# Kernel tuning notes

Measured on AMD Instinct MI355X. Metric: run time of the kernel, lower is better.

## Reference

```python
import jax, jax.numpy as jnp
import numpy as np

# Dimensions: D must equal C_CHUNK**2 (original code's view+transpose requires it)
D = 4096        # flattened input dim per sample
C_CHUNK = 64    # chunk_size (rows of G per chunk)
N_CHUNKS = D // C_CHUNK  # = 64
H = 512         # hidden dim of forward_func MLP
C_OUT = 8       # output classes of forward_func
B = 8           # batch size (state_batch has 2*B rows)
EPS_G = 1e-4    # metric regularizer (constant under grad)


def setup_inputs() -> dict:
    key = jax.random.key(0)
    ks = jax.random.split(key, 6)
    t = jax.random.uniform(ks[0], (1,), dtype=jnp.float32)
    state_batch = jax.random.normal(ks[1], (2 * B, D), dtype=jnp.float32)
    x0_batch = jax.random.normal(ks[2], (B, D), dtype=jnp.float32)
    x1_batch = jax.random.normal(ks[3], (B, D), dtype=jnp.float32)
    W1 = jax.random.normal(ks[4], (D, H), dtype=jnp.float32) / np.float32(np.sqrt(D))
    W2 = jax.random.normal(ks[5], (H, C_OUT), dtype=jnp.float32) / np.float32(np.sqrt(H))
    return {"t": t, "state_batch": state_batch, "x0_batch": x0_batch,
            "x1_batch": x1_batch, "W1": W1, "W2": W2}


def _accel_per_sample(x, v, W1, W2):
    """Chunked Christoffel-symbol contraction for one sample.
    x: [D] current point, v: [D] deviation velocity. Returns a: [D]."""
    def f(xi):  # forward_func: 2-layer tanh MLP, [D] -> [C_OUT]
        return jnp.tanh(xi @ W1) @ W2

    ones = jnp.ones((D,), x.dtype)

    def chunk_sums(xi):
        # G = J^T J + eps*I; row_sums[i] = sum_j G[i,j] computed without
        # materializing the D x D metric: J^T (J @ 1)  (+ const eps on diag).
        J = jax.jacrev(f)(xi)              # [C_OUT, D]
        row = J.T @ (J @ ones)             # [D]
        return row.reshape(N_CHUNKS, C_CHUNK).sum(axis=1)  # [N_CHUNKS]

    g = jax.jacrev(chunk_sums)(x)          # [N_CHUNKS, D] = dG_chunk_sum/dx
    g = g.reshape(N_CHUNKS, C_CHUNK, C_CHUNK)
    g = g / (jnp.linalg.norm(g, axis=2, keepdims=True) + 1e-6)
    Gamma = 0.5 * (g + jnp.swapaxes(g, 1, 2))   # symmetrized [nc, c, c]
    vc = v.reshape(N_CHUNKS, C_CHUNK)
    # a_chunk[i] = -sum_k Gamma[i,k] v_i v_k  (Christoffel quadratic in v)
    a = -jnp.einsum('nik,ni,nk->ni', Gamma, vc, vc)
    return a.reshape(D)


def reference(t, state_batch, x0_batch, x1_batch, W1, W2):
    ts = t[0]
    Bn = state_batch.shape[0] // 2
    deviation = state_batch[:Bn]
    dev_velocity = state_batch[Bn:]
    window = 4.0 * ts * (1.0 - ts)
    x = x0_batch + ts * (x1_batch - x0_batch) + window * deviation  # [B, D]
    a = jax.vmap(_accel_per_sample, in_axes=(0, 0, None, None))(x, dev_velocity, W1, W2)
    a = a / (jnp.linalg.norm(dev_velocity, axis=1, keepdims=True) + 1e-6)
    restoration = -0.1 * deviation
    return jnp.concatenate([dev_velocity, a + restoration], axis=0)  # [2B, D]
```

## Files before the change

### kernel.cpp

```cpp
#include <hip/hip_runtime.h>

#define D 4096
#define H 512
#define NCH 64
#define CCH 64
#define B 8
#define COUT 8

typedef __bf16 bf16x8 __attribute__((ext_vector_type(8)));
typedef float  f32x4  __attribute__((ext_vector_type(4)));

#define OFF_P    0
#define OFF_PHN  (OFF_P + NCH*H)
#define OFF_UPT  (OFF_PHN + H*NCH)
#define OFF_S    (OFF_UPT + B*H*NCH)
#define OFF_ST2  (OFF_S + B*H)
#define OFF_Q    (OFF_ST2 + B*H)
#define OFF_C    (OFF_Q + B*H)
#define OFF_VN   (OFF_C + H)
#define OFF_A1   (OFF_VN + 64)
#define OFF_ZB   (OFF_A1 + B*NCH*CCH)
#define OFF_W1H  (OFF_ZB + B*64*4096)
#define OFF_W1L  (OFF_W1H + (D*H)/2)
#define OFF_WH   (OFF_W1L + (D*H)/2)
#define OFF_WL   (OFF_WH + (B*NCH*H)/2)

__device__ __forceinline__ unsigned short f2bf(float x) {
    unsigned int u = __float_as_uint(x);
    unsigned int r = (u + 0x7FFFu + ((u >> 16) & 1u)) >> 16;
    return (unsigned short)r;
}
__device__ __forceinline__ float bf2f(unsigned short s) {
    return __uint_as_float(((unsigned int)s) << 16);
}

__global__ __launch_bounds__(256) void k1_reduce_w1(const float* __restrict__ W1,
                                                    const float* __restrict__ state,
                                                    const float* __restrict__ x0,
                                                    const float* __restrict__ x1,
                                                    const float* __restrict__ tptr,
                                                    float* __restrict__ ws) {
    int n   = blockIdx.x;
    int ht  = blockIdx.y;
    int tid = threadIdx.x;
    int hq  = ht * 32 + (tid & 31);
    int jh  = tid >> 5;

    __shared__ float xs[B][64];
    __shared__ f32x4 red[8][32][9];

    float ts = tptr[0];
    float window = 4.f * ts * (1.f - ts);
    if (tid < 64) {
        int d = n * 64 + tid;
        for (int b = 0; b < B; ++b) {
            float a0 = x0[b * D + d];
            float a1v = x1[b * D + d];
            float dev = state[b * D + d];
            xs[b][tid] = a0 + ts * (a1v - a0) + window * dev;
        }
    }
    __syncthreads();

    unsigned short* __restrict__ W1Hp = (unsigned short*)(ws + OFF_W1H);
    unsigned short* __restrict__ W1Lp = (unsigned short*)(ws + OFF_W1L);

    f32x4 p4 = {0.f, 0.f, 0.f, 0.f};
    f32x4 up[B];
#pragma unroll
    for (int b = 0; b < B; ++b) up[b] = p4;

#pragma unroll
    for (int jj = 0; jj < 8; ++jj) {
        int j = jh * 8 + jj;
        int d = n * 64 + j;
        f32x4 w = ((const f32x4*)W1)[d * (H / 4) + hq];
        p4 += w;
#pragma unroll
        for (int b = 0; b < B; ++b) up[b] += w * xs[b][j];
        unsigned short h0 = f2bf(w.x), h1 = f2bf(w.y), h2 = f2bf(w.z), h3 = f2bf(w.w);
        ushort4 hv = {h0, h1, h2, h3};
        ushort4 lv = {f2bf(w.x - bf2f(h0)), f2bf(w.y - bf2f(h1)),
                      f2bf(w.z - bf2f(h2)), f2bf(w.w - bf2f(h3))};
        *(ushort4*)(W1Hp + d * H + hq * 4) = hv;
        *(ushort4*)(W1Lp + d * H + hq * 4) = lv;
    }

    int l = tid & 31;
    red[jh][l][0] = p4;
#pragma unroll
    for (int b = 0; b < B; ++b) red[jh][l][1 + b] = up[b];
    __syncthreads();

    if (jh == 0) {
        f32x4 pt = red[0][l][0];
        f32x4 ut[B];
#pragma unroll
        for (int b = 0; b < B; ++b) ut[b] = red[0][l][1 + b];
        for (int g = 1; g < 8; ++g) {
            pt += red[g][l][0];
#pragma unroll
            for (int b = 0; b < B; ++b) ut[b] += red[g][l][1 + b];
        }
        *(f32x4*)(ws + OFF_P + n * H + hq * 4) = pt;
#pragma unroll
        for (int e = 0; e < 4; ++e) ws[OFF_PHN + (hq * 4 + e) * NCH + n] = pt[e];
#pragma unroll
        for (int b = 0; b < B; ++b)
#pragma unroll
            for (int e = 0; e < 4; ++e)
                ws[OFF_UPT + (b * H + hq * 4 + e) * NCH + n] = ut[b][e];
    }
}

__global__ void k2_sample(const float* __restrict__ W2,
                          const float* __restrict__ state,
                          float* __restrict__ ws) {
    int b = blockIdx.x, tid = threadIdx.x;
    int wid = tid >> 6, lane = tid & 63;
    __shared__ float lm[8][8];
    __shared__ float ms[8];
    __shared__ float lv[8];

    int h = tid;
    f32x4 u4 = {0.f, 0.f, 0.f, 0.f}, c4 = u4;
    const f32x4* upp = (const f32x4*)(ws + OFF_UPT + (b * H + h) * NCH);
    const f32x4* pp  = (const f32x4*)(ws + OFF_PHN + h * NCH);
#pragma unroll
    for (int j = 0; j < 16; ++j) { u4 += upp[j]; c4 += pp[j]; }
    float u = u4.x + u4.y + u4.z + u4.w;
    float c = c4.x + c4.y + c4.z + c4.w;

    float tt  = tanhf(u);
    float s   = 1.f - tt * tt;
    float st2 = -2.f * tt * s;
    ws[OFF_S   + b * H + h] = s;
    ws[OFF_ST2 + b * H + h] = st2;
    ws[OFF_C   + h] = c;

    const float4* w2p = (const float4*)(W2 + h * 8);
    float4 w2a = w2p[0], w2b = w2p[1];
    float w2r[8] = {w2a.x, w2a.y, w2a.z, w2a.w, w2b.x, w2b.y, w2b.z, w2b.w};

    float cs = c * s;
    float pr[8];
#pragma unroll
    for (int o = 0; o < 8; ++o) pr[o] = cs * w2r[o];
#pragma unroll
    for (int mk = 1; mk < 64; mk <<= 1)
#pragma unroll
        for (int o = 0; o < 8; ++o) pr[o] += __shfl_xor(pr[o], mk);
    if (lane == 0)
#pragma unroll
        for (int o = 0; o < 8; ++o) lm[wid][o] = pr[o];

    float v2 = 0.f;
    const float* v = state + (size_t)(B + b) * D;
#pragma unroll
    for (int j = 0; j < D / H; ++j) { float vv = v[j * H + h]; v2 += vv * vv; }
#pragma unroll
    for (int mk = 1; mk < 64; mk <<= 1) v2 += __shfl_xor(v2, mk);
    if (lane == 0) lv[wid] = v2;
    __syncthreads();

    if (tid < 8) {
        float a = 0.f;
        for (int w = 0; w < 8; ++w) a += lm[w][tid];
        ms[tid] = a;
    }
    if (tid == 0) {
        float a = 0.f;
        for (int w = 0; w < 8; ++w) a += lv[w];
        ws[OFF_VN + b] = sqrtf(a) + 1e-6f;
    }
    __syncthreads();

    float q = 0.f;
#pragma unroll
    for (int o = 0; o < 8; ++o) q += w2r[o] * ms[o];
    ws[OFF_Q + b * H + h] = q;
}

__global__ void k3_w(const float* __restrict__ W2,
                     float* __restrict__ ws) {
    int n = blockIdx.x, b = blockIdx.y, lane = threadIdx.x;
    float M[8];
#pragma unroll
    for (int o = 0; o < 8; ++o) M[o] = 0.f;
    for (int j = 0; j < 8; ++j) {
        int h = j * 64 + lane;
        float ps = ws[OFF_P + n * H + h] * ws[OFF_S + b * H + h];
        const float4* wp = (const float4*)(W2 + h * 8);
        float4 wa = wp[0], wb = wp[1];
        M[0] += ps * wa.x; M[1] += ps * wa.y; M[2] += ps * wa.z; M[3] += ps * wa.w;
        M[4] += ps * wb.x; M[5] += ps * wb.y; M[6] += ps * wb.z; M[7] += ps * wb.w;
    }
#pragma unroll
    for (int mk = 1; mk < 64; mk <<= 1)
#pragma unroll
        for (int o = 0; o < 8; ++o) M[o] += __shfl_xor(M[o], mk);

    unsigned short* __restrict__ WHp = (unsigned short*)(ws + OFF_WH);
    unsigned short* __restrict__ WLp = (unsigned short*)(ws + OFF_WL);
    for (int j = 0; j < 8; ++j) {
        int h = j * 64 + lane;
        const float4* wp = (const float4*)(W2 + h * 8);
        float4 wa = wp[0], wb = wp[1];
        float r = wa.x*M[0] + wa.y*M[1] + wa.z*M[2] + wa.w*M[3]
                + wb.x*M[4] + wb.y*M[5] + wb.z*M[6] + wb.w*M[7];
        float P = ws[OFF_P + n * H + h];
        float wv = ws[OFF_ST2 + b * H + h] * (P * ws[OFF_Q + b * H + h] + ws[OFF_C + h] * r);
        unsigned short hi = f2bf(wv);
        WHp[(b * NCH + n) * H + h] = hi;
        WLp[(b * NCH + n) * H + h] = f2bf(wv - bf2f(hi));
    }
}

__global__ __launch_bounds__(256) void k4_mfma(const float* __restrict__ state,
                                               float* __restrict__ ws) {
    int i   = blockIdx.x;
    int b   = blockIdx.y;
    int tid = threadIdx.x;
    int wid = tid >> 6, lane = tid & 63;
    int r16 = lane & 15;
    int kgrp = (lane >> 4) * 8;

    __shared__ float gp[2][64][67];
    __shared__ float coefs[64];

    const unsigned short* __restrict__ W1Hp = (const unsigned short*)(ws + OFF_W1H);
    const unsigned short* __restrict__ W1Lp = (const unsigned short*)(ws + OFF_W1L);
    const unsigned short* __restrict__ WHp  = (const unsigned short*)(ws + OFF_WH);
    const unsigned short* __restrict__ WLp  = (const unsigned short*)(ws + OFF_WL);

    f32x4 acc[4][4];
    f32x4 z4 = {0.f, 0.f, 0.f, 0.f};
#pragma unroll
    for (int m = 0; m < 4; ++m)
#pragma unroll
        for (int c = 0; c < 4; ++c) acc[m][c] = z4;

    int kb = wid * 128 + kgrp;
#pragma unroll
    for (int ks = 0; ks < 4; ++ks) {
        int k = kb + ks * 32;
        bf16x8 ah[4], al[4], bh[4], bl[4];
#pragma unroll
        for (int m = 0; m < 4; ++m) {
            int off = (b * 64 + m * 16 + r16) * H + k;
            ah[m] = *(const bf16x8*)(WHp + off);
            al[m] = *(const bf16x8*)(WLp + off);
        }
#pragma unroll
        for (int c = 0; c < 4; ++c) {
            int off = (i * 64 + c * 16 + r16) * H + k;
            bh[c] = *(const bf16x8*)(W1Hp + off);
            bl[c] = *(const bf16x8*)(W1Lp + off);
        }
#pragma unroll
        for (int m = 0; m < 4; ++m)
#pragma unroll
            for (int c = 0; c < 4; ++c) {
                acc[m][c] = __builtin_amdgcn_mfma_f32_16x16x32_bf16(ah[m], bh[c], acc[m][c], 0, 0, 0);
                acc[m][c] = __builtin_amdgcn_mfma_f32_16x16x32_bf16(ah[m], bl[c], acc[m][c], 0, 0, 0);
                acc[m][c] = __builtin_amdgcn_mfma_f32_16x16x32_bf16(al[m], bh[c], acc[m][c], 0, 0, 0);
            }
    }

    int rowb = (lane >> 4) * 4;
    if (wid < 2) {
        float (*g)[67] = gp[wid];
#pragma unroll
        for (int m = 0; m < 4; ++m)
#pragma unroll
            for (int c = 0; c < 4; ++c)
#pragma unroll
                for (int e = 0; e < 4; ++e)
                    g[m * 16 + rowb + e][c * 16 + r16] = acc[m][c][e];
    }
    __syncthreads();
    if (wid >= 2) {
        float (*g)[67] = gp[wid - 2];
#pragma unroll
        for (int m = 0; m < 4; ++m)
#pragma unroll
            for (int c = 0; c < 4; ++c)
#pragma unroll
                for (int e = 0; e < 4; ++e)
                    g[m * 16 + rowb + e][c * 16 + r16] += acc[m][c][e];
    }
    __syncthreads();

    const float* v = state + (size_t)(B + b) * D;

    if (tid < 64) {
        int n = tid;
        float ss = 0.f, y = 0.f;
#pragma unroll 8
        for (int k = 0; k < 64; ++k) {
            float g = gp[0][n][k] + gp[1][n][k];
            ss += g * g;
            y  += g * v[n * 64 + k];
        }
        float nrm = sqrtf(ss) + 1e-6f;
        ws[OFF_A1 + (size_t)(b * NCH + n) * CCH + i] = y / nrm;
        coefs[n] = v[n * 64 + i] / nrm;
    }
    __syncthreads();

    float* zb = ws + OFF_ZB + ((size_t)b * 64 + i) * 4096;
#pragma unroll
    for (int r = 0; r < 16; ++r) {
        int idx = tid + r * 256;
        int n = idx >> 6, k = idx & 63;
        zb[idx] = (gp[0][n][k] + gp[1][n][k]) * coefs[n];
    }
}

__global__ void k5_final(const float* __restrict__ state,
                         const float* __restrict__ ws,
                         float* __restrict__ out) {
    int idx = blockIdx.x * 256 + threadIdx.x;
    float vel = state[32768 + idx];
    out[idx] = vel;
    int b = idx >> 12, e = idx & 4095;
    const float* zb = ws + OFF_ZB + (size_t)b * 64 * 4096 + e;
    float z = 0.f;
#pragma unroll 8
    for (int i = 0; i < 64; ++i) z += zb[(size_t)i * 4096];
    float a1 = ws[OFF_A1 + (size_t)b * 4096 + e];
    float av = -0.5f * vel * (a1 + z) / ws[OFF_VN + b];
    out[32768 + idx] = av - 0.1f * state[idx];
}

extern "C" void kernel_launch(void* const* d_in, const int* in_sizes, int n_in,
                              void* d_out, int out_size, void* d_ws, size_t ws_size,
                              hipStream_t stream) {
    const float* t   = (const float*)d_in[0];
    const float* st  = (const float*)d_in[1];
    const float* x0  = (const float*)d_in[2];
    const float* x1  = (const float*)d_in[3];
    const float* W1  = (const float*)d_in[4];
    const float* W2  = (const float*)d_in[5];
    float* out = (float*)d_out;
    float* ws  = (float*)d_ws;

    hipLaunchKernelGGL(k1_reduce_w1, dim3(64, 4), dim3(256), 0, stream, W1, st, x0, x1, t, ws);
    hipLaunchKernelGGL(k2_sample,    dim3(8),     dim3(512), 0, stream, W2, st, ws);
    hipLaunchKernelGGL(k3_w,         dim3(64, 8), dim3(64),  0, stream, W2, ws);
    hipLaunchKernelGGL(k4_mfma,      dim3(64, 8), dim3(256), 0, stream, st, ws);
    hipLaunchKernelGGL(k5_final,     dim3(128),   dim3(256), 0, stream, st, ws, out);
}
```

Before: 121.8 us.

## Fuse five kernels into one cooperative kernel with grid syncs

```diff
diff --git a/kernel.cpp b/kernel.cpp
--- a/kernel.cpp
+++ b/kernel.cpp
@@ -1,11 +1,13 @@
 #include <hip/hip_runtime.h>
+#include <hip/hip_cooperative_groups.h>
+
+namespace cg = cooperative_groups;
 
 #define D 4096
 #define H 512
 #define NCH 64
 #define CCH 64
 #define B 8
-#define COUT 8
 
 typedef __bf16 bf16x8 __attribute__((ext_vector_type(8)));
 typedef float  f32x4  __attribute__((ext_vector_type(4)));
@@ -34,303 +36,310 @@
     return __uint_as_float(((unsigned int)s) << 16);
 }
 
-__global__ __launch_bounds__(256) void k1_reduce_w1(const float* __restrict__ W1,
-                                                    const float* __restrict__ state,
-                                                    const float* __restrict__ x0,
-                                                    const float* __restrict__ x1,
-                                                    const float* __restrict__ tptr,
-                                                    float* __restrict__ ws) {
-    int n   = blockIdx.x;
-    int ht  = blockIdx.y;
+__global__ __launch_bounds__(512, 2)
+void fused(const float* __restrict__ W1, const float* __restrict__ state,
+           const float* __restrict__ x0, const float* __restrict__ x1,
+           const float* __restrict__ tptr, const float* __restrict__ W2,
+           float* __restrict__ ws, float* __restrict__ out) {
+    cg::grid_group grid = cg::this_grid();
+    int bid = blockIdx.x;
     int tid = threadIdx.x;
-    int hq  = ht * 32 + (tid & 31);
-    int jh  = tid >> 5;
-
-    __shared__ float xs[B][64];
-    __shared__ f32x4 red[8][32][9];
-
-    float ts = tptr[0];
-    float window = 4.f * ts * (1.f - ts);
-    if (tid < 64) {
-        int d = n * 64 + tid;
-        for (int b = 0; b < B; ++b) {
-            float a0 = x0[b * D + d];
-            float a1v = x1[b * D + d];
-            float dev = state[b * D + d];
-            xs[b][tid] = a0 + ts * (a1v - a0) + window * dev;
-        }
-    }
-    __syncthreads();
+
+    __shared__ union {
+        struct { float xs[B][64]; f32x4 red[8][32][9]; } p1;
+        struct { float lm[8][8]; float ms[8]; float lv[8]; } p2;
+        struct { float gp[2][2][64][67]; float coefs[2][64]; } p4;
+    } sh;
 
     unsigned short* __restrict__ W1Hp = (unsigned short*)(ws + OFF_W1H);
     unsigned short* __restrict__ W1Lp = (unsigned short*)(ws + OFF_W1L);
-
-    f32x4 p4 = {0.f, 0.f, 0.f, 0.f};
-    f32x4 up[B];
-#pragma unroll
-    for (int b = 0; b < B; ++b) up[b] = p4;
-
-#pragma unroll
-    for (int jj = 0; jj < 8; ++jj) {
-        int j = jh * 8 + jj;
-        int d = n * 64 + j;
-        f32x4 w = ((const f32x4*)W1)[d * (H / 4) + hq];
-        p4 += w;
-#pragma unroll
-        for (int b = 0; b < B; ++b) up[b] += w * xs[b][j];
-        unsigned short h0 = f2bf(w.x), h1 = f2bf(w.y), h2 = f2bf(w.z), h3 = f2bf(w.w);
-        ushort4 hv = {h0, h1, h2, h3};
-        ushort4 lv = {f2bf(w.x - bf2f(h0)), f2bf(w.y - bf2f(h1)),
-                      f2bf(w.z - bf2f(h2)), f2bf(w.w - bf2f(h3))};
-        *(ushort4*)(W1Hp + d * H + hq * 4) = hv;
-        *(ushort4*)(W1Lp + d * H + hq * 4) = lv;
-    }
-
-    int l = tid & 31;
-    red[jh][l][0] = p4;
-#pragma unroll
-    for (int b = 0; b < B; ++b) red[jh][l][1 + b] = up[b];
-    __syncthreads();
-
-    if (jh == 0) {
-        f32x4 pt = red[0][l][0];
-        f32x4 ut[B];
-#pragma unroll
-        for (int b = 0; b < B; ++b) ut[b] = red[0][l][1 + b];
-        for (int g = 1; g < 8; ++g) {
-            pt += red[g][l][0];
-#pragma unroll
-            for (int b = 0; b < B; ++b) ut[b] += red[g][l][1 + b];
-        }
-        *(f32x4*)(ws + OFF_P + n * H + hq * 4) = pt;
-#pragma unroll
-        for (int e = 0; e < 4; ++e) ws[OFF_PHN + (hq * 4 + e) * NCH + n] = pt[e];
-#pragma unroll
-        for (int b = 0; b < B; ++b)
-#pragma unroll
-            for (int e = 0; e < 4; ++e)
-                ws[OFF_UPT + (b * H + hq * 4 + e) * NCH + n] = ut[b][e];
-    }
-}
-
-__global__ void k2_sample(const float* __restrict__ W2,
-                          const float* __restrict__ state,
-                          float* __restrict__ ws) {
-    int b = blockIdx.x, tid = threadIdx.x;
-    int wid = tid >> 6, lane = tid & 63;
-    __shared__ float lm[8][8];
-    __shared__ float ms[8];
-    __shared__ float lv[8];
-
-    int h = tid;
-    f32x4 u4 = {0.f, 0.f, 0.f, 0.f}, c4 = u4;
-    const f32x4* upp = (const f32x4*)(ws + OFF_UPT + (b * H + h) * NCH);
-    const f32x4* pp  = (const f32x4*)(ws + OFF_PHN + h * NCH);
-#pragma unroll
-    for (int j = 0; j < 16; ++j) { u4 += upp[j]; c4 += pp[j]; }
-    float u = u4.x + u4.y + u4.z + u4.w;
-    float c = c4.x + c4.y + c4.z + c4.w;
-
-    float tt  = tanhf(u);
-    float s   = 1.f - tt * tt;
-    float st2 = -2.f * tt * s;
-    ws[OFF_S   + b * H + h] = s;
-    ws[OFF_ST2 + b * H + h] = st2;
-    ws[OFF_C   + h] = c;
-
-    const float4* w2p = (const float4*)(W2 + h * 8);
-    float4 w2a = w2p[0], w2b = w2p[1];
-    float w2r[8] = {w2a.x, w2a.y, w2a.z, w2a.w, w2b.x, w2b.y, w2b.z, w2b.w};
-
-    float cs = c * s;
-    float pr[8];
-#pragma unroll
-    for (int o = 0; o < 8; ++o) pr[o] = cs * w2r[o];
-#pragma unroll
-    for (int mk = 1; mk < 64; mk <<= 1)
-#pragma unroll
-        for (int o = 0; o < 8; ++o) pr[o] += __shfl_xor(pr[o], mk);
-    if (lane == 0)
-#pragma unroll
-        for (int o = 0; o < 8; ++o) lm[wid][o] = pr[o];
-
-    float v2 = 0.f;
-    const float* v = state + (size_t)(B + b) * D;
-#pragma unroll
-    for (int j = 0; j < D / H; ++j) { float vv = v[j * H + h]; v2 += vv * vv; }
-#pragma unroll
-    for (int mk = 1; mk < 64; mk <<= 1) v2 += __shfl_xor(v2, mk);
-    if (lane == 0) lv[wid] = v2;
-    __syncthreads();
-
-    if (tid < 8) {
-        float a = 0.f;
-        for (int w = 0; w < 8; ++w) a += lm[w][tid];
-        ms[tid] = a;
-    }
-    if (tid == 0) {
-        float a = 0.f;
-        for (int w = 0; w < 8; ++w) a += lv[w];
-        ws[OFF_VN + b] = sqrtf(a) + 1e-6f;
-    }
-    __syncthreads();
-
-    float q = 0.f;
-#pragma unroll
-    for (int o = 0; o < 8; ++o) q += w2r[o] * ms[o];
-    ws[OFF_Q + b * H + h] = q;
-}
-
-__global__ void k3_w(const float* __restrict__ W2,
-                     float* __restrict__ ws) {
-    int n = blockIdx.x, b = blockIdx.y, lane = threadIdx.x;
-    float M[8];
-#pragma unroll
-    for (int o = 0; o < 8; ++o) M[o] = 0.f;
-    for (int j = 0; j < 8; ++j) {
-        int h = j * 64 + lane;
-        float ps = ws[OFF_P + n * H + h] * ws[OFF_S + b * H + h];
-        const float4* wp = (const float4*)(W2 + h * 8);
-        float4 wa = wp[0], wb = wp[1];
-        M[0] += ps * wa.x; M[1] += ps * wa.y; M[2] += ps * wa.z; M[3] += ps * wa.w;
-        M[4] += ps * wb.x; M[5] += ps * wb.y; M[6] += ps * wb.z; M[7] += ps * wb.w;
-    }
-#pragma unroll
-    for (int mk = 1; mk < 64; mk <<= 1)
-#pragma unroll
-        for (int o = 0; o < 8; ++o) M[o] += __shfl_xor(M[o], mk);
-
-    unsigned short* __restrict__ WHp = (unsigned short*)(ws + OFF_WH);
-    unsigned short* __restrict__ WLp = (unsigned short*)(ws + OFF_WL);
-    for (int j = 0; j < 8; ++j) {
-        int h = j * 64 + lane;
-        const float4* wp = (const float4*)(W2 + h * 8);
-        float4 wa = wp[0], wb = wp[1];
-        float r = wa.x*M[0] + wa.y*M[1] + wa.z*M[2] + wa.w*M[3]
-                + wb.x*M[4] + wb.y*M[5] + wb.z*M[6] + wb.w*M[7];
-        float P = ws[OFF_P + n * H + h];
-        float wv = ws[OFF_ST2 + b * H + h] * (P * ws[OFF_Q + b * H + h] + ws[OFF_C + h] * r);
-        unsigned short hi = f2bf(wv);
-        WHp[(b * NCH + n) * H + h] = hi;
-        WLp[(b * NCH + n) * H + h] = f2bf(wv - bf2f(hi));
-    }
-}
-
-__global__ __launch_bounds__(256) void k4_mfma(const float* __restrict__ state,
-                                               float* __restrict__ ws) {
-    int i   = blockIdx.x;
-    int b   = blockIdx.y;
-    int tid = threadIdx.x;
-    int wid = tid >> 6, lane = tid & 63;
-    int r16 = lane & 15;
-    int kgrp = (lane >> 4) * 8;
-
-    __shared__ float gp[2][64][67];
-    __shared__ float coefs[64];
-
-    const unsigned short* __restrict__ W1Hp = (const unsigned short*)(ws + OFF_W1H);
-    const unsigned short* __restrict__ W1Lp = (const unsigned short*)(ws + OFF_W1L);
-    const unsigned short* __restrict__ WHp  = (const unsigned short*)(ws + OFF_WH);
-    const unsigned short* __restrict__ WLp  = (const unsigned short*)(ws + OFF_WL);
-
-    f32x4 acc[4][4];
-    f32x4 z4 = {0.f, 0.f, 0.f, 0.f};
-#pragma unroll
-    for (int m = 0; m < 4; ++m)
-#pragma unroll
-        for (int c = 0; c < 4; ++c) acc[m][c] = z4;
-
-    int kb = wid * 128 + kgrp;
-#pragma unroll
-    for (int ks = 0; ks < 4; ++ks) {
-        int k = kb + ks * 32;
-        bf16x8 ah[4], al[4], bh[4], bl[4];
-#pragma unroll
-        for (int m = 0; m < 4; ++m) {
-            int off = (b * 64 + m * 16 + r16) * H + k;
-            ah[m] = *(const bf16x8*)(WHp + off);
-            al[m] = *(const bf16x8*)(WLp + off);
-        }
-#pragma unroll
-        for (int c = 0; c < 4; ++c) {
-            int off = (i * 64 + c * 16 + r16) * H + k;
-            bh[c] = *(const bf16x8*)(W1Hp + off);
-            bl[c] = *(const bf16x8*)(W1Lp + off);
-        }
+    unsigned short* __restrict__ WHp  = (unsigned short*)(ws + OFF_WH);
+    unsigned short* __restrict__ WLp  = (unsigned short*)(ws + OFF_WL);
+
+    {
+        int n = bid >> 2, ht = bid & 3;
+        float ts = tptr[0];
+        float window = 4.f * ts * (1.f - ts);
+        if (tid < 64) {
+            int d = n * 64 + tid;
+            for (int b = 0; b < B; ++b) {
+                float a0 = x0[b * D + d];
+                float a1v = x1[b * D + d];
+                float dev = state[b * D + d];
+                sh.p1.xs[b][tid] = a0 + ts * (a1v - a0) + window * dev;
+            }
+        }
+        __syncthreads();
+
+        if (tid < 256) {
+            int hq = ht * 32 + (tid & 31);
+            int jh = tid >> 5;
+            f32x4 p4v = {0.f, 0.f, 0.f, 0.f};
+            f32x4 up[B];
+#pragma unroll
+            for (int b = 0; b < B; ++b) up[b] = p4v;
+#pragma unroll
+            for (int jj = 0; jj < 8; ++jj) {
+                int j = jh * 8 + jj;
+                int d = n * 64 + j;
+                f32x4 w = ((const f32x4*)W1)[d * (H / 4) + hq];
+                p4v += w;
+#pragma unroll
+                for (int b = 0; b < B; ++b) up[b] += w * sh.p1.xs[b][j];
+                unsigned short h0 = f2bf(w.x), h1 = f2bf(w.y), h2 = f2bf(w.z), h3 = f2bf(w.w);
+                ushort4 hv = {h0, h1, h2, h3};
+                ushort4 lv = {f2bf(w.x - bf2f(h0)), f2bf(w.y - bf2f(h1)),
+                              f2bf(w.z - bf2f(h2)), f2bf(w.w - bf2f(h3))};
+                *(ushort4*)(W1Hp + d * H + hq * 4) = hv;
+                *(ushort4*)(W1Lp + d * H + hq * 4) = lv;
+            }
+            int l = tid & 31;
+            sh.p1.red[jh][l][0] = p4v;
+#pragma unroll
+            for (int b = 0; b < B; ++b) sh.p1.red[jh][l][1 + b] = up[b];
+        }
+        __syncthreads();
+
+        if (tid < 32) {
+            int l = tid;
+            int hq = ht * 32 + l;
+            f32x4 pt = sh.p1.red[0][l][0];
+            f32x4 ut[B];
+#pragma unroll
+            for (int b = 0; b < B; ++b) ut[b] = sh.p1.red[0][l][1 + b];
+            for (int g = 1; g < 8; ++g) {
+                pt += sh.p1.red[g][l][0];
+#pragma unroll
+                for (int b = 0; b < B; ++b) ut[b] += sh.p1.red[g][l][1 + b];
+            }
+            *(f32x4*)(ws + OFF_P + n * H + hq * 4) = pt;
+#pragma unroll
+            for (int e = 0; e < 4; ++e) ws[OFF_PHN + (hq * 4 + e) * NCH + n] = pt[e];
+#pragma unroll
+            for (int b = 0; b < B; ++b)
+#pragma unroll
+                for (int e = 0; e < 4; ++e)
+                    ws[OFF_UPT + (b * H + hq * 4 + e) * NCH + n] = ut[b][e];
+        }
+    }
+    grid.sync();
+
+    if (bid < 8) {
+        int b = bid;
+        int wid = tid >> 6, lane = tid & 63;
+        int h = tid;
+        f32x4 u4 = {0.f, 0.f, 0.f, 0.f}, c4 = u4;
+        const f32x4* upp = (const f32x4*)(ws + OFF_UPT + (b * H + h) * NCH);
+        const f32x4* pp  = (const f32x4*)(ws + OFF_PHN + h * NCH);
+#pragma unroll
+        for (int j = 0; j < 16; ++j) { u4 += upp[j]; c4 += pp[j]; }
+        float u = u4.x + u4.y + u4.z + u4.w;
+        float c = c4.x + c4.y + c4.z + c4.w;
+
+        float tt  = tanhf(u);
+        float s   = 1.f - tt * tt;
+        float st2 = -2.f * tt * s;
+        ws[OFF_S   + b * H + h] = s;
+        ws[OFF_ST2 + b * H + h] = st2;
+        ws[OFF_C   + h] = c;
+
+        const float4* w2p = (const float4*)(W2 + h * 8);
+        float4 w2a = w2p[0], w2b = w2p[1];
+        float w2r[8] = {w2a.x, w2a.y, w2a.z, w2a.w, w2b.x, w2b.y, w2b.z, w2b.w};
+
+        float cs = c * s;
+        float pr[8];
+#pragma unroll
+        for (int o = 0; o < 8; ++o) pr[o] = cs * w2r[o];
+#pragma unroll
+        for (int mk = 1; mk < 64; mk <<= 1)
+#pragma unroll
+            for (int o = 0; o < 8; ++o) pr[o] += __shfl_xor(pr[o], mk);
+        if (lane == 0)
+#pragma unroll
+            for (int o = 0; o < 8; ++o) sh.p2.lm[wid][o] = pr[o];
+
+        float v2 = 0.f;
+        const float* v = state + (size_t)(B + b) * D;
+#pragma unroll
+        for (int j = 0; j < D / H; ++j) { float vv = v[j * H + h]; v2 += vv * vv; }
+#pragma unroll
+        for (int mk = 1; mk < 64; mk <<= 1) v2 += __shfl_xor(v2, mk);
+        if (lane == 0) sh.p2.lv[wid] = v2;
+        __syncthreads();
+
+        if (tid < 8) {
+            float a = 0.f;
+            for (int w = 0; w < 8; ++w) a += sh.p2.lm[w][tid];
+            sh.p2.ms[tid] = a;
+        }
+        if (tid == 0) {
+            float a = 0.f;
+            for (int w = 0; w < 8; ++w) a += sh.p2.lv[w];
+            ws[OFF_VN + b] = sqrtf(a) + 1e-6f;
+        }
+        __syncthreads();
+
+        float q = 0.f;
+#pragma unroll
+        for (int o = 0; o < 8; ++o) q += w2r[o] * sh.p2.ms[o];
+        ws[OFF_Q + b * H + h] = q;
+    }
+    grid.sync();
+
+    {
+        int gw = bid * 8 + (tid >> 6);
+        if (gw < 512) {
+            int n = gw >> 3, b = gw & 7;
+            int lane = tid & 63;
+            float M[8];
+#pragma unroll
+            for (int o = 0; o < 8; ++o) M[o] = 0.f;
+            for (int j = 0; j < 8; ++j) {
+                int h = j * 64 + lane;
+                float ps = ws[OFF_P + n * H + h] * ws[OFF_S + b * H + h];
+                const float4* wp = (const float4*)(W2 + h * 8);
+                float4 wa = wp[0], wb = wp[1];
+                M[0] += ps * wa.x; M[1] += ps * wa.y; M[2] += ps * wa.z; M[3] += ps * wa.w;
+                M[4] += ps * wb.x; M[5] += ps * wb.y; M[6] += ps * wb.z; M[7] += ps * wb.w;
+            }
+#pragma unroll
+            for (int mk = 1; mk < 64; mk <<= 1)
+#pragma unroll
+                for (int o = 0; o < 8; ++o) M[o] += __shfl_xor(M[o], mk);
+
+            for (int j = 0; j < 8; ++j) {
+                int h = j * 64 + lane;
+                const float4* wp = (const float4*)(W2 + h * 8);
+                float4 wa = wp[0], wb = wp[1];
+                float r = wa.x*M[0] + wa.y*M[1] + wa.z*M[2] + wa.w*M[3]
+                        + wb.x*M[4] + wb.y*M[5] + wb.z*M[6] + wb.w*M[7];
+                float P = ws[OFF_P + n * H + h];
+                float wv = ws[OFF_ST2 + b * H + h] * (P * ws[OFF_Q + b * H + h] + ws[OFF_C + h] * r);
+                unsigned short hi = f2bf(wv);
+                WHp[(b * NCH + n) * H + h] = hi;
+                WLp[(b * NCH + n) * H + h] = f2bf(wv - bf2f(hi));
+            }
+        }
+    }
+    grid.sync();
+
+    {
+        int g    = tid >> 8;
+        int gt   = tid & 255;
+        int u    = bid * 2 + g;
+        int i    = u >> 3, b = u & 7;
+        int w2   = gt >> 6;
+        int lane = tid & 63;
+        int r16  = lane & 15;
+        int kgrp = (lane >> 4) * 8;
+
+        f32x4 acc[4][4];
+        f32x4 zz = {0.f, 0.f, 0.f, 0.f};
 #pragma unroll
         for (int m = 0; m < 4; ++m)
 #pragma unroll
-            for (int c = 0; c < 4; ++c) {
-                acc[m][c] = __builtin_amdgcn_mfma_f32_16x16x32_bf16(ah[m], bh[c], acc[m][c], 0, 0, 0);
-                acc[m][c] = __builtin_amdgcn_mfma_f32_16x16x32_bf16(ah[m], bl[c], acc[m][c], 0, 0, 0);
-                acc[m][c] = __builtin_amdgcn_mfma_f32_16x16x32_bf16(al[m], bh[c], acc[m][c], 0, 0, 0);
-            }
-    }
-
-    int rowb = (lane >> 4) * 4;
-    if (wid < 2) {
-        float (*g)[67] = gp[wid];
-#pragma unroll
-        for (int m = 0; m < 4; ++m)
-#pragma unroll
-            for (int c = 0; c < 4; ++c)
-#pragma unroll
-                for (int e = 0; e < 4; ++e)
-                    g[m * 16 + rowb + e][c * 16 + r16] = acc[m][c][e];
-    }
-    __syncthreads();
-    if (wid >= 2) {
-        float (*g)[67] = gp[wid - 2];
-#pragma unroll
-        for (int m = 0; m < 4; ++m)
-#pragma unroll
-            for (int c = 0; c < 4; ++c)
-#pragma unroll
-                for (int e = 0; e < 4; ++e)
-                    g[m * 16 + rowb + e][c * 16 + r16] += acc[m][c][e];
-    }
-    __syncthreads();
-
-    const float* v = state + (size_t)(B + b) * D;
-
-    if (tid < 64) {
-        int n = tid;
-        float ss = 0.f, y = 0.f;
+            for (int c = 0; c < 4; ++c) acc[m][c] = zz;
+
+        int kb = w2 * 128 + kgrp;
+        int baseA = (b * 64 + r16) * H;
+        int baseB = (i * 64 + r16) * H;
+
+        bf16x8 fa[2][8], fb[2][8];
+#define LOADF(BUF, KOFS) do {                                              \
+        int k_ = (KOFS);                                                   \
+        _Pragma("unroll")                                                  \
+        for (int m_ = 0; m_ < 4; ++m_) {                                   \
+            int oA = baseA + m_ * 16 * H + k_;                             \
+            fa[BUF][m_]     = *(const bf16x8*)(WHp + oA);                  \
+            fa[BUF][4 + m_] = *(const bf16x8*)(WLp + oA);                  \
+            int oB = baseB + m_ * 16 * H + k_;                             \
+            fb[BUF][m_]     = *(const bf16x8*)(W1Hp + oB);                 \
+            fb[BUF][4 + m_] = *(const bf16x8*)(W1Lp + oB);                 \
+        } } while (0)
+
+        LOADF(0, kb);
+#pragma unroll
+        for (int ks = 0; ks < 4; ++ks) {
+            int cur = ks & 1;
+            if (ks < 3) {
+                if (cur == 0) LOADF(1, kb + (ks + 1) * 32);
+                else          LOADF(0, kb + (ks + 1) * 32);
+            }
+#pragma unroll
+            for (int m = 0; m < 4; ++m)
+#pragma unroll
+                for (int c = 0; c < 4; ++c) {
+                    acc[m][c] = __builtin_amdgcn_mfma_f32_16x16x32_bf16(fa[cur][m], fb[cur][c], acc[m][c], 0, 0, 0);
+                    acc[m][c] = __builtin_amdgcn_mfma_f32_16x16x32_bf16(fa[cur][m], fb[cur][4 + c], acc[m][c], 0, 0, 0);
+                    acc[m][c] = __builtin_amdgcn_mfma_f32_16x16x32_bf16(fa[cur][4 + m], fb[cur][c], acc[m][c], 0, 0, 0);
+                }
+        }
+#undef LOADF
+
+        int rowb = (lane >> 4) * 4;
+        if (w2 < 2) {
+            float (*gpp)[67] = sh.p4.gp[g][w2];
+#pragma unroll
+            for (int m = 0; m < 4; ++m)
+#pragma unroll
+                for (int c = 0; c < 4; ++c)
+#pragma unroll
+                    for (int e = 0; e < 4; ++e)
+                        gpp[m * 16 + rowb + e][c * 16 + r16] = acc[m][c][e];
+        }
+        __syncthreads();
+        if (w2 >= 2) {
+            float (*gpp)[67] = sh.p4.gp[g][w2 - 2];
+#pragma unroll
+            for (int m = 0; m < 4; ++m)
+#pragma unroll
+                for (int c = 0; c < 4; ++c)
+#pragma unroll
+                    for (int e = 0; e < 4; ++e)
+                        gpp[m * 16 + rowb + e][c * 16 + r16] += acc[m][c][e];
+        }
+        __syncthreads();
+
+        const float* v = state + (size_t)(B + b) * D;
+        if (gt < 64) {
+            int n = gt;
+            float ss = 0.f, y = 0.f;
 #pragma unroll 8
-        for (int k = 0; k < 64; ++k) {
-            float g = gp[0][n][k] + gp[1][n][k];
-            ss += g * g;
-            y  += g * v[n * 64 + k];
-        }
-        float nrm = sqrtf(ss) + 1e-6f;
-        ws[OFF_A1 + (size_t)(b * NCH + n) * CCH + i] = y / nrm;
-        coefs[n] = v[n * 64 + i] / nrm;
-    }
-    __syncthreads();
-
-    float* zb = ws + OFF_ZB + ((size_t)b * 64 + i) * 4096;
-#pragma unroll
-    for (int r = 0; r < 16; ++r) {
-        int idx = tid + r * 256;
-        int n = idx >> 6, k = idx & 63;
-        zb[idx] = (gp[0][n][k] + gp[1][n][k]) * coefs[n];
-    }
-}
-
-__global__ void k5_final(const float* __restrict__ state,
-                         const float* __restrict__ ws,
-                         float* __restrict__ out) {
-    int idx = blockIdx.x * 256 + threadIdx.x;
-    float vel = state[32768 + idx];
-    out[idx] = vel;
-    int b = idx >> 12, e = idx & 4095;
-    const float* zb = ws + OFF_ZB + (size_t)b * 64 * 4096 + e;
-    float z = 0.f;
+            for (int k = 0; k < 64; ++k) {
+                float gv = sh.p4.gp[g][0][n][k] + sh.p4.gp[g][1][n][k];
+                ss += gv * gv;
+                y  += gv * v[n * 64 + k];
+            }
+            float nrm = sqrtf(ss) + 1e-6f;
+            ws[OFF_A1 + (size_t)(b * NCH + n) * CCH + i] = y / nrm;
+            sh.p4.coefs[g][n] = v[n * 64 + i] / nrm;
+        }
+        __syncthreads();
+
+        float* zb = ws + OFF_ZB + ((size_t)b * 64 + i) * 4096;
+#pragma unroll
+        for (int r = 0; r < 16; ++r) {
+            int idx = gt + r * 256;
+            int n = idx >> 6, k = idx & 63;
+            zb[idx] = (sh.p4.gp[g][0][n][k] + sh.p4.gp[g][1][n][k]) * sh.p4.coefs[g][n];
+        }
+    }
+    grid.sync();
+
+    if (bid < 64) {
+        int idx = bid * 512 + tid;
+        float vel = state[32768 + idx];
+        out[idx] = vel;
+        int b = idx >> 12, e = idx & 4095;
+        const float* zb = ws + OFF_ZB + (size_t)b * 64 * 4096 + e;
+        float z = 0.f;
 #pragma unroll 8
-    for (int i = 0; i < 64; ++i) z += zb[(size_t)i * 4096];
-    float a1 = ws[OFF_A1 + (size_t)b * 4096 + e];
-    float av = -0.5f * vel * (a1 + z) / ws[OFF_VN + b];
-    out[32768 + idx] = av - 0.1f * state[idx];
+        for (int i = 0; i < 64; ++i) z += zb[(size_t)i * 4096];
+        float a1 = ws[OFF_A1 + (size_t)b * 4096 + e];
+        float av = -0.5f * vel * (a1 + z) / ws[OFF_VN + b];
+        out[32768 + idx] = av - 0.1f * state[idx];
+    }
 }
 
 extern "C" void kernel_launch(void* const* d_in, const int* in_sizes, int n_in,
@@ -345,9 +354,8 @@
     float* out = (float*)d_out;
     float* ws  = (float*)d_ws;
 
-    hipLaunchKernelGGL(k1_reduce_w1, dim3(64, 4), dim3(256), 0, stream, W1, st, x0, x1, t, ws);
-    hipLaunchKernelGGL(k2_sample,    dim3(8),     dim3(512), 0, stream, W2, st, ws);
-    hipLaunchKernelGGL(k3_w,         dim3(64, 8), dim3(64),  0, stream, W2, ws);
-    hipLaunchKernelGGL(k4_mfma,      dim3(64, 8), dim3(256), 0, stream, st, ws);
-    hipLaunchKernelGGL(k5_final,     dim3(128),   dim3(256), 0, stream, st, ws, out);
+    void* args[] = {(void*)&W1, (void*)&st, (void*)&x0, (void*)&x1,
+                    (void*)&t, (void*)&W2, (void*)&ws, (void*)&out};
+    hipLaunchCooperativeKernel((const void*)fused, dim3(256), dim3(512),
+                               args, 0, stream);
 }
```

Measured after the change: 253.6 us. +108.2%, slower.
